# Kernel optimization log

Measured on AMD Instinct MI355X. Metric: run time of the kernel, lower is better.

Reference implementation:

```python
import jax, jax.numpy as jnp
import numpy as np

B, T, H, DH = 4, 2048, 16, 64   # batch, block_size, num_head, chunk_size (per-head dim)
NE = H * DH                      # n_embed = 1024
EPS = 1e-5                       # torch GroupNorm default eps


def _decay_mask(T):
    # D[h, n, m] = gamma_h**(n-m) for n>=m else 0 (RetNet decay matrix)
    gamma = 1.0 - 2.0 ** (-5.0 - jnp.arange(H, dtype=jnp.float32))  # [H]
    idx = jnp.arange(T)
    diff = idx[:, None] - idx[None, :]                # [T, T]
    mask = diff >= 0
    expo = jnp.where(mask, diff, 0).astype(jnp.float32)
    D = (gamma[:, None, None] ** expo[None]) * mask[None].astype(jnp.float32)
    return gamma, D


def setup_inputs() -> dict:
    key = jax.random.key(0)
    ks = jax.random.split(key, 5)
    x = jax.random.normal(ks[0], (B, T, NE), jnp.float32)
    past_kv = jax.random.normal(ks[1], (H, DH, DH), jnp.float32)
    Wq = jax.random.normal(ks[2], (NE, NE), jnp.float32) * 0.02
    Wk = jax.random.normal(ks[3], (NE, NE), jnp.float32) * 0.02
    Wv = jax.random.normal(ks[4], (NE, NE), jnp.float32) * 0.02
    gn_w = jnp.ones((H,), jnp.float32)
    gn_b = jnp.zeros((H,), jnp.float32)
    return {"x": x, "past_kv": past_kv, "Wq": Wq, "Wk": Wk, "Wv": Wv,
            "gn_w": gn_w, "gn_b": gn_b}


def reference(x, past_kv, Wq, Wk, Wv, gn_w, gn_b):
    b, t, c = x.shape
    gamma, D = _decay_mask(t)                                  # [H], [H,T,T]

    def split_heads(y):
        return y.reshape(b, t, H, DH).transpose(0, 2, 1, 3)    # [B,H,T,DH]

    q = split_heads(x @ Wq)
    k = split_heads(x @ Wk)
    v = split_heads(x @ Wv)

    # intra-chunk retention: (Q K^T) * D
    retention = jnp.einsum('bhtd,bhsd->bhts', q, k) * D[None]  # [B,H,T,T]
    inner = jnp.einsum('bhts,bhsd->bhtd', retention, v)        # [B,H,T,DH]

    # cross-chunk term (faithful to source): ((q @ past_kv)^T @ D)^T
    pp = jnp.einsum('bhtd,hde->bhte', q, past_kv)              # [B,H,T,DH]
    cross = jnp.einsum('hst,bhse->bhte', D, pp)                # [B,H,T,DH]

    ret = inner + cross                                        # [B,H,T,DH]

    # GroupNorm(1, H) over channels-first layout [B, H, DH, T]
    y = ret.transpose(0, 1, 3, 2)                              # [B,H,DH,T]
    mu = y.mean(axis=(1, 2, 3), keepdims=True)
    var = y.var(axis=(1, 2, 3), keepdims=True)                 # biased, as torch
    yn = (y - mu) / jnp.sqrt(var + EPS)
    yn = yn * gn_w[None, :, None, None] + gn_b[None, :, None, None]

    # rearrange 'b c h t -> b t (c h)' with (c=H, h=DH)
    out = yn.transpose(0, 3, 1, 2).reshape(b, t, H * DH)       # [B,T,NE]

    # recurrent state update: gamma * past_kv + K^T V, batch-averaged
    current_kv = gamma[:, None, None] * past_kv[None] + \
                 jnp.einsum('bhtd,bhte->bhde', k, v)           # [B,H,DH,DH]
    return out, current_kv.mean(axis=0)
```

## Files before the change

### kernel.cpp

```cpp
#include <hip/hip_runtime.h>
#include <stdint.h>

typedef float v4f __attribute__((ext_vector_type(4)));
typedef short v8s __attribute__((ext_vector_type(8)));

#define SZ_BHTD 8388608
#define SZ_HTD  131072

#define GL2LDS(g, l) __builtin_amdgcn_global_load_lds( \
    (const __attribute__((address_space(1))) void*)(g), \
    (__attribute__((address_space(3))) void*)(l), 16, 0, 0)

__device__ __forceinline__ uint16_t f2bf(float f){
  uint32_t u = __float_as_uint(f);
  u += 0x7fffu + ((u >> 16) & 1u);
  return (uint16_t)(u >> 16);
}
__device__ __forceinline__ float bf2f(uint16_t v){
  return __uint_as_float(((uint32_t)v) << 16);
}

__global__ __launch_bounds__(256) void k_conv(const float* __restrict__ x,
                                              const float* __restrict__ Wq, const float* __restrict__ Wk,
                                              const float* __restrict__ Wv,
                                              uint16_t* __restrict__ xb, uint16_t* __restrict__ wt){
  if (blockIdx.x < 8192){
    int i = blockIdx.x*256 + threadIdx.x;
    const float4 v = ((const float4*)x)[i];
    ushort4 o; o.x = f2bf(v.x); o.y = f2bf(v.y); o.z = f2bf(v.z); o.w = f2bf(v.w);
    ((ushort4*)xb)[i] = o;
    return;
  }
  __shared__ float t[64][65];
  const int blk2 = blockIdx.x - 8192;
  const int z = blk2 >> 8, y = (blk2 >> 4) & 15, xx = blk2 & 15;
  const float* W = z==0 ? Wq : (z==1 ? Wk : Wv);
  int n0 = xx*64, k0 = y*64;
  for (int idx = threadIdx.x; idx < 4096; idx += 256){
    int r = idx >> 6, c = idx & 63;
    t[r][c] = W[(k0+r)*1024 + n0 + c];
  }
  __syncthreads();
  for (int idx = threadIdx.x; idx < 4096; idx += 256){
    int r = idx >> 6, c = idx & 63;
    wt[(size_t)(z*1024 + n0 + r)*1024 + k0 + c] = f2bf(t[c][r]);
  }
}

__global__ __launch_bounds__(256) void k_gemm(const uint16_t* __restrict__ Xb, const uint16_t* __restrict__ Wt,
                                              uint16_t* __restrict__ qkv){
  __shared__ uint16_t As[128*64];
  __shared__ uint16_t Bs[128*64];
  const int tid = threadIdx.x;
  const int lane = tid & 63, w = tid >> 6;
  const int quad = lane >> 4, l16 = lane & 15;
  const int wm = (w >> 1)*64, wn = (w & 1)*64;
  const int bm = blockIdx.x, bn = blockIdx.y;
  v4f acc[4][4] = {};
  const uint16_t* Ag = Xb + (size_t)(bm*128)*1024;
  const uint16_t* Bg = Wt + (size_t)(bn*128)*1024;
  const int rA = lane >> 3;
  const int ce = (((lane & 7) ^ rA) * 8);
  const int xr = l16 & 7;
  for (int k0 = 0; k0 < 1024; k0 += 64){
    #pragma unroll
    for (int j = 0; j < 4; ++j){
      const int cA = w*4 + j;
      const int r = cA*8 + rA;
      GL2LDS(Ag + (size_t)r*1024 + k0 + ce, As + cA*512);
      GL2LDS(Bg + (size_t)r*1024 + k0 + ce, Bs + cA*512);
    }
    __syncthreads();
    #pragma unroll
    for (int kk = 0; kk < 64; kk += 32){
      const int ch = ((quad + (kk >> 3)) ^ xr) * 8;
      v8s a[4], b[4];
      #pragma unroll
      for (int u = 0; u < 4; ++u) a[u] = *(v8s*)&As[(wm + u*16 + l16)*64 + ch];
      #pragma unroll
      for (int u = 0; u < 4; ++u) b[u] = *(v8s*)&Bs[(wn + u*16 + l16)*64 + ch];
      #pragma unroll
      for (int mi = 0; mi < 4; ++mi)
        #pragma unroll
        for (int ni = 0; ni < 4; ++ni)
          acc[mi][ni] = __builtin_amdgcn_mfma_f32_16x16x32_bf16(a[mi], b[ni], acc[mi][ni], 0, 0, 0);
    }
    __syncthreads();
  }
  #pragma unroll
  for (int mi = 0; mi < 4; ++mi){
    #pragma unroll
    for (int ni = 0; ni < 4; ++ni){
      int n = bn*128 + wn + ni*16 + l16;
      int which = n >> 10, cch = n & 1023;
      int hh = cch >> 6, dd = cch & 63;
      #pragma unroll
      for (int r = 0; r < 4; ++r){
        int m = bm*128 + wm + mi*16 + quad*4 + r;
        int b = m >> 11, t = m & 2047;
        qkv[(size_t)which*SZ_BHTD + (size_t)((b*16 + hh)*2048 + t)*64 + dd] = f2bf(acc[mi][ni][r]);
      }
    }
  }
}

__global__ __launch_bounds__(256) void k_pre(const uint16_t* __restrict__ qkv, const float* __restrict__ pkv,
                                             uint16_t* __restrict__ UT, uint16_t* __restrict__ ckp,
                                             float* __restrict__ headv){
  __shared__ uint16_t KTb[64*72];
  __shared__ uint16_t VTb[64*72];
  __shared__ uint16_t VTw[64*72];
  __shared__ float tab[65];
  __shared__ float qbar[64];
  const int tid = threadIdx.x, blk = blockIdx.x;
  const int bh = blk >> 5, c = blk & 31, h = bh & 15;
  const int lane = tid & 63, w = tid >> 6;
  const int quad = lane >> 4, l16 = lane & 15;
  const float g = 1.0f - exp2f(-(float)(5 + h));
  if (tid <= 64) tab[tid] = powf(g, (float)tid);
  const uint16_t* Qg = qkv + (size_t)bh*SZ_HTD + c*4096;
  const uint16_t* Kg = Qg + SZ_BHTD;
  const uint16_t* Vg = Qg + 2*(size_t)SZ_BHTD;
  const float* Pg = pkv + h*4096;
  __syncthreads();
  #pragma unroll
  for (int it = 0; it < 16; ++it){
    int idx = it*256 + tid;
    int s = idx >> 6, d = idx & 63;
    uint16_t kv = Kg[idx], vv = Vg[idx];
    KTb[d*72 + s] = kv;
    VTb[d*72 + s] = vv;
    VTw[d*72 + s] = f2bf(tab[63 - s]*bf2f(vv));
  }
  if (tid < 64){
    float acc = 0.f;
    for (int j = 0; j < 64; ++j) acc = fmaf(tab[j], bf2f(Qg[j*64 + tid]), acc);
    qbar[tid] = acc;
  }
  __syncthreads();
  const int ar = (w*16 + l16)*72 + quad*8;
  v8s aK0 = *(v8s*)&KTb[ar], aK1 = *(v8s*)&KTb[ar + 32];
  v8s aW0 = *(v8s*)&VTw[ar], aW1 = *(v8s*)&VTw[ar + 32];
  v4f accC[4] = {}, accU[4] = {};
  #pragma unroll
  for (int ni = 0; ni < 4; ++ni){
    const int br = (ni*16 + l16)*72 + quad*8;
    v8s bV0 = *(v8s*)&VTb[br], bV1 = *(v8s*)&VTb[br + 32];
    v8s bK0 = *(v8s*)&KTb[br], bK1 = *(v8s*)&KTb[br + 32];
    accC[ni] = __builtin_amdgcn_mfma_f32_16x16x32_bf16(aK0, bV0, accC[ni], 0, 0, 0);
    accC[ni] = __builtin_amdgcn_mfma_f32_16x16x32_bf16(aK1, bV1, accC[ni], 0, 0, 0);
    accU[ni] = __builtin_amdgcn_mfma_f32_16x16x32_bf16(aW0, bK0, accU[ni], 0, 0, 0);
    accU[ni] = __builtin_amdgcn_mfma_f32_16x16x32_bf16(aW1, bK1, accU[ni], 0, 0, 0);
  }
  const size_t ob = (size_t)blk*4096;
  #pragma unroll
  for (int ni = 0; ni < 4; ++ni){
    int e = ni*16 + l16;
    #pragma unroll
    for (int r = 0; r < 4; ++r){
      int d = w*16 + quad*4 + r;
      ckp[ob + d*64 + e] = f2bf(accC[ni][r]);
      UT[ob + d*64 + e]  = f2bf(accU[ni][r]);
    }
  }
  if (tid < 64){
    float acc = 0.f;
    for (int dd = 0; dd < 64; ++dd) acc = fmaf(qbar[dd], Pg[dd*64 + tid], acc);
    headv[(size_t)blk*64 + tid] = acc;
  }
}

__global__ __launch_bounds__(256) void k_scan(const uint16_t* __restrict__ UT, uint16_t* __restrict__ S,
                                              const float* __restrict__ headv, float* __restrict__ tailv){
  if (blockIdx.x < 256){
    const int bh = blockIdx.x >> 2, part = blockIdx.x & 3, h = bh & 15;
    const float g = 1.0f - exp2f(-(float)(5 + h));
    const float g64 = powf(g, 64.0f);
    const int off = part*1024 + threadIdx.x*4;
    float st0=0.f, st1=0.f, st2=0.f, st3=0.f;
    for (int c = 0; c < 32; ++c){
      const size_t base = ((size_t)bh*32 + c)*4096 + off;
      ushort4 u = *(const ushort4*)&UT[base];
      ushort4 o; o.x=f2bf(st0); o.y=f2bf(st1); o.z=f2bf(st2); o.w=f2bf(st3);
      *(ushort4*)&S[base] = o;
      st0 = fmaf(g64, st0, bf2f(u.x)); st1 = fmaf(g64, st1, bf2f(u.y));
      st2 = fmaf(g64, st2, bf2f(u.z)); st3 = fmaf(g64, st3, bf2f(u.w));
    }
    return;
  }
  const int lin = (blockIdx.x - 256)*256 + threadIdx.x;
  const int bh = lin >> 6, e = lin & 63, h = bh & 15;
  const float g = 1.0f - exp2f(-(float)(5 + h));
  const float g64 = powf(g, 64.0f);
  float R = 0.0f;
  for (int c = 31; c >= 0; --c){
    const size_t o = ((size_t)bh*32 + c)*64 + e;
    tailv[o] = R;
    R = fmaf(g64, R, headv[o]);
  }
}

__global__ __launch_bounds__(256) void k_main(const uint16_t* __restrict__ qkv, const uint16_t* __restrict__ Sg_,
                                              const float* __restrict__ pkv, const float* __restrict__ tailv,
                                              uint16_t* __restrict__ ret, float2* __restrict__ pb){
  __shared__ uint16_t Qb[64*72];
  __shared__ uint16_t Kb[64*72];
  __shared__ uint16_t VTb[64*72];
  __shared__ uint16_t B2[64*72];
  __shared__ uint16_t Sb[64*72];
  __shared__ float tab[65];
  __shared__ float ps[8];
  const int tid = threadIdx.x, blk = blockIdx.x;
  const int bh = blk >> 5, c = blk & 31, h = bh & 15;
  const int lane = tid & 63, w = tid >> 6;
  const int quad = lane >> 4, l16 = lane & 15;
  const float g = 1.0f - exp2f(-(float)(5 + h));
  if (tid <= 64) tab[tid] = powf(g, (float)tid);
  const uint16_t* Qg = qkv + (size_t)bh*SZ_HTD + c*4096;
  const uint16_t* Kg = Qg + SZ_BHTD;
  const uint16_t* Vg = Qg + 2*(size_t)SZ_BHTD;
  const uint16_t* Sgp = Sg_ + (size_t)blk*4096;
  const float* Pg = pkv + h*4096;
  #pragma unroll
  for (int v = 0; v < 2; ++v){
    int idx = (tid*2 + v)*8;
    int r = idx >> 6, cc = idx & 63;
    *(uint4*)&Qb[r*72 + cc] = *(const uint4*)&Qg[idx];
    *(uint4*)&Kb[r*72 + cc] = *(const uint4*)&Kg[idx];
    *(uint4*)&Sb[r*72 + cc] = *(const uint4*)&Sgp[idx];
  }
  #pragma unroll
  for (int it = 0; it < 16; ++it){
    int idx = it*256 + tid;
    int r = idx >> 6, cc = idx & 63;
    VTb[cc*72 + r] = Vg[idx];
    B2[cc*72 + r] = f2bf(Pg[idx]);
  }
  __syncthreads();
  const int ar = (w*16 + l16)*72 + quad*8;
  v8s aQ0 = *(v8s*)&Qb[ar], aQ1 = *(v8s*)&Qb[ar + 32];
  v4f accP[4] = {}, accPP[4] = {}, accIT[4] = {};
  #pragma unroll
  for (int ni = 0; ni < 4; ++ni){
    const int br = (ni*16 + l16)*72 + quad*8;
    v8s b0 = *(v8s*)&Kb[br], b1 = *(v8s*)&Kb[br + 32];
    accP[ni] = __builtin_amdgcn_mfma_f32_16x16x32_bf16(aQ0, b0, accP[ni], 0, 0, 0);
    accP[ni] = __builtin_amdgcn_mfma_f32_16x16x32_bf16(aQ1, b1, accP[ni], 0, 0, 0);
    v8s c0 = *(v8s*)&B2[br], c1 = *(v8s*)&B2[br + 32];
    accPP[ni] = __builtin_amdgcn_mfma_f32_16x16x32_bf16(aQ0, c0, accPP[ni], 0, 0, 0);
    accPP[ni] = __builtin_amdgcn_mfma_f32_16x16x32_bf16(aQ1, c1, accPP[ni], 0, 0, 0);
    v8s d0 = *(v8s*)&Sb[br], d1 = *(v8s*)&Sb[br + 32];
    accIT[ni] = __builtin_amdgcn_mfma_f32_16x16x32_bf16(aQ0, d0, accIT[ni], 0, 0, 0);
    accIT[ni] = __builtin_amdgcn_mfma_f32_16x16x32_bf16(aQ1, d1, accIT[ni], 0, 0, 0);
  }
  __syncthreads();
  #pragma unroll
  for (int ni = 0; ni < 4; ++ni){
    #pragma unroll
    for (int r = 0; r < 4; ++r){
      int i = w*16 + quad*4 + r;
      int j = ni*16 + l16;
      Kb[i*72 + j] = f2bf((i >= j) ? accP[ni][r]*tab[i - j] : 0.0f);
      B2[j*72 + i] = f2bf(accPP[ni][r]);
    }
  }
  __syncthreads();
  v8s aP0 = *(v8s*)&Kb[ar], aP1 = *(v8s*)&Kb[ar + 32];
  v8s aM0, aM1;
  {
    int i = w*16 + l16;
    #pragma unroll
    for (int u = 0; u < 8; ++u){
      int j0 = quad*8 + u, j1 = 32 + quad*8 + u;
      aM0[u] = (short)f2bf((j0 >= i) ? tab[j0 - i] : 0.0f);
      aM1[u] = (short)f2bf((j1 >= i) ? tab[j1 - i] : 0.0f);
    }
  }
  v4f accI[4] = {}, accX[4] = {};
  #pragma unroll
  for (int ni = 0; ni < 4; ++ni){
    const int br = (ni*16 + l16)*72 + quad*8;
    v8s b0 = *(v8s*)&VTb[br], b1 = *(v8s*)&VTb[br + 32];
    accI[ni] = __builtin_amdgcn_mfma_f32_16x16x32_bf16(aP0, b0, accI[ni], 0, 0, 0);
    accI[ni] = __builtin_amdgcn_mfma_f32_16x16x32_bf16(aP1, b1, accI[ni], 0, 0, 0);
    v8s e0 = *(v8s*)&B2[br], e1 = *(v8s*)&B2[br + 32];
    accX[ni] = __builtin_amdgcn_mfma_f32_16x16x32_bf16(aM0, e0, accX[ni], 0, 0, 0);
    accX[ni] = __builtin_amdgcn_mfma_f32_16x16x32_bf16(aM1, e1, accX[ni], 0, 0, 0);
  }
  const size_t rbase = (size_t)bh*2048 + (size_t)c*64;
  float s1 = 0.f, s2 = 0.f;
  #pragma unroll
  for (int ni = 0; ni < 4; ++ni){
    int d = ni*16 + l16;
    float tl = tailv[(size_t)blk*64 + d];
    #pragma unroll
    for (int r = 0; r < 4; ++r){
      int i = w*16 + quad*4 + r;
      float v = accI[ni][r] + tab[i + 1]*accIT[ni][r] + accX[ni][r] + tab[64 - i]*tl;
      ret[(rbase + i)*64 + d] = f2bf(v);
      s1 += v; s2 += v*v;
    }
  }
  #pragma unroll
  for (int off = 32; off > 0; off >>= 1){
    s1 += __shfl_down(s1, off);
    s2 += __shfl_down(s2, off);
  }
  if (lane == 0){ ps[w*2] = s1; ps[w*2+1] = s2; }
  __syncthreads();
  if (tid == 0){
    float2 o; o.x = ps[0] + ps[2] + ps[4] + ps[6];
    o.y = ps[1] + ps[3] + ps[5] + ps[7];
    pb[blk] = o;
  }
}

__global__ __launch_bounds__(256) void k_stats(const float2* __restrict__ pb, float* __restrict__ stats){
  __shared__ float ps[8];
  const int b = blockIdx.x;
  float s = 0.0f, s2 = 0.0f;
  for (int i = threadIdx.x; i < 512; i += 256){
    const float2 p = pb[(size_t)b*512 + i];
    s += p.x; s2 += p.y;
  }
  #pragma unroll
  for (int off = 32; off > 0; off >>= 1){
    s  += __shfl_down(s, off);
    s2 += __shfl_down(s2, off);
  }
  const int wv = threadIdx.x >> 6;
  if ((threadIdx.x & 63) == 0){ ps[wv*2] = s; ps[wv*2+1] = s2; }
  __syncthreads();
  if (threadIdx.x == 0){
    stats[b*2]   = ps[0] + ps[2] + ps[4] + ps[6];
    stats[b*2+1] = ps[1] + ps[3] + ps[5] + ps[7];
  }
}

__global__ __launch_bounds__(256) void k_norm(const uint16_t* __restrict__ ret, const float* __restrict__ stats,
                                              const float* __restrict__ gw, const float* __restrict__ gb,
                                              float* __restrict__ out){
  const int o = (blockIdx.x*256 + threadIdx.x)*4;
  const int b = o >> 21, t = (o >> 10) & 2047, cch = o & 1023;
  const int h = cch >> 6, d = cch & 63;
  const float inv = 1.0f/2097152.0f;
  const float mu = stats[b*2]*inv;
  const float var = stats[b*2+1]*inv - mu*mu;
  const float rs = rsqrtf(var + 1e-5f);
  const float w = gw[h]*rs, bb = gb[h];
  const ushort4 v = *(const ushort4*)&ret[((size_t)(b*16 + h)*2048 + t)*64 + d];
  float4 r;
  r.x = (bf2f(v.x) - mu)*w + bb; r.y = (bf2f(v.y) - mu)*w + bb;
  r.z = (bf2f(v.z) - mu)*w + bb; r.w = (bf2f(v.w) - mu)*w + bb;
  *(float4*)&out[o] = r;
}

__global__ __launch_bounds__(256) void k_ckb(const float* __restrict__ pkv, const uint16_t* __restrict__ ckp,
                                             float* __restrict__ out2){
  const int lin = blockIdx.x*256 + threadIdx.x;
  const int i = lin*4;
  const int h = i >> 12, de = i & 4095;
  const float g = 1.0f - exp2f(-(float)(5 + h));
  float acc[4] = {0.0f, 0.0f, 0.0f, 0.0f};
  for (int b = 0; b < 4; ++b){
    const uint16_t* base = ckp + ((size_t)(b*16 + h)*32)*4096 + de;
    for (int c = 0; c < 32; ++c){
      #pragma unroll
      for (int u = 0; u < 4; ++u) acc[u] += bf2f(base[(size_t)c*4096 + u]);
    }
  }
  #pragma unroll
  for (int u = 0; u < 4; ++u)
    out2[i + u] = fmaf(g, pkv[i + u], 0.25f*acc[u]);
}

extern "C" void kernel_launch(void* const* d_in, const int* in_sizes, int n_in,
                              void* d_out, int out_size, void* d_ws, size_t ws_size,
                              hipStream_t stream){
  const float* x   = (const float*)d_in[0];
  const float* pkv = (const float*)d_in[1];
  const float* Wq  = (const float*)d_in[2];
  const float* Wk  = (const float*)d_in[3];
  const float* Wv  = (const float*)d_in[4];
  const float* gnw = (const float*)d_in[5];
  const float* gnb = (const float*)d_in[6];
  float* out  = (float*)d_out;
  float* out2 = out + 8388608;

  char* ws = (char*)d_ws;
  size_t off = 0;
  float*    stats = (float*)(ws + off);    off += 256;
  float2*   pb    = (float2*)(ws + off);   off += (size_t)8192*8;
  uint16_t* Xb    = (uint16_t*)(ws + off); off += (size_t)8388608*2;
  uint16_t* Wt    = (uint16_t*)(ws + off); off += (size_t)3145728*2;
  uint16_t* QKV   = (uint16_t*)(ws + off); off += (size_t)3*8388608*2;
  uint16_t* ret   = (uint16_t*)(ws + off); off += (size_t)8388608*2;
  uint16_t* UT    = (uint16_t*)(ws + off); off += (size_t)8388608*2;
  uint16_t* S     = (uint16_t*)(ws + off); off += (size_t)8388608*2;
  uint16_t* CKp   = (uint16_t*)(ws + off); off += (size_t)8388608*2;
  float*    headv = (float*)(ws + off);    off += (size_t)131072*4;
  float*    tailv = (float*)(ws + off);    off += (size_t)131072*4;

  k_conv<<<8960, 256, 0, stream>>>(x, Wq, Wk, Wv, Xb, Wt);
  k_gemm<<<dim3(64, 24), 256, 0, stream>>>(Xb, Wt, QKV);
  k_pre<<<2048, 256, 0, stream>>>(QKV, pkv, UT, CKp, headv);
  k_scan<<<272, 256, 0, stream>>>(UT, S, headv, tailv);
  k_main<<<2048, 256, 0, stream>>>(QKV, S, pkv, tailv, ret, pb);
  k_stats<<<4, 256, 0, stream>>>(pb, stats);
  k_norm<<<8192, 256, 0, stream>>>(ret, stats, gnw, gnb, out);
  k_ckb<<<64, 256, 0, stream>>>(pkv, CKp, out2);
}
```

Baseline: 252.5 us.

## Rewrite QKV GEMM as 256x256 double-buffered tile with 8 waves; spread k_ckb

The QKV projection GEMM moves from 128x128 tiles with 4 waves to 256x256 tiles with 8 waves. LDS is double-buffered, so the global-to-LDS loads for tile k+2 overlap the MFMA work on the current tile, using explicit vmcnt waits, raw barriers and s_setprio around the MFMA bursts. The aim is more data reuse per tile and hiding load latency, at the cost of far fewer blocks (384), more LDS and more registers. k_ckb is also relaunched as 256 blocks of 64 threads to spread its reduction over more CUs.

```diff
diff --git a/kernel.cpp b/kernel.cpp
--- a/kernel.cpp
+++ b/kernel.cpp
@@ -10,6 +10,8 @@
 #define GL2LDS(g, l) __builtin_amdgcn_global_load_lds( \
     (const __attribute__((address_space(1))) void*)(g), \
     (__attribute__((address_space(3))) void*)(l), 16, 0, 0)
+
+#define BAR() do{ asm volatile("" ::: "memory"); __builtin_amdgcn_s_barrier(); asm volatile("" ::: "memory"); }while(0)
 
 __device__ __forceinline__ uint16_t f2bf(float f){
   uint32_t u = __float_as_uint(f);
@@ -47,58 +49,97 @@
   }
 }
 
-__global__ __launch_bounds__(256) void k_gemm(const uint16_t* __restrict__ Xb, const uint16_t* __restrict__ Wt,
-                                              uint16_t* __restrict__ qkv){
-  __shared__ uint16_t As[128*64];
-  __shared__ uint16_t Bs[128*64];
+#define NT 16
+__global__ __launch_bounds__(512, 2) void k_gemm(const uint16_t* __restrict__ Xb, const uint16_t* __restrict__ Wt,
+                                                 uint16_t* __restrict__ qkv){
+  __shared__ uint16_t As[2][256*64];
+  __shared__ uint16_t Bs[2][256*64];
   const int tid = threadIdx.x;
   const int lane = tid & 63, w = tid >> 6;
   const int quad = lane >> 4, l16 = lane & 15;
-  const int wm = (w >> 1)*64, wn = (w & 1)*64;
+  const int wm = w >> 2, wn = w & 3;
   const int bm = blockIdx.x, bn = blockIdx.y;
-  v4f acc[4][4] = {};
-  const uint16_t* Ag = Xb + (size_t)(bm*128)*1024;
-  const uint16_t* Bg = Wt + (size_t)(bn*128)*1024;
+  const uint16_t* Ag = Xb + (size_t)(bm*256)*1024;
+  const uint16_t* Bg = Wt + (size_t)(bn*256)*1024;
   const int rA = lane >> 3;
   const int ce = (((lane & 7) ^ rA) * 8);
   const int xr = l16 & 7;
-  for (int k0 = 0; k0 < 1024; k0 += 64){
-    #pragma unroll
-    for (int j = 0; j < 4; ++j){
-      const int cA = w*4 + j;
-      const int r = cA*8 + rA;
-      GL2LDS(Ag + (size_t)r*1024 + k0 + ce, As + cA*512);
-      GL2LDS(Bg + (size_t)r*1024 + k0 + ce, Bs + cA*512);
-    }
-    __syncthreads();
-    #pragma unroll
-    for (int kk = 0; kk < 64; kk += 32){
-      const int ch = ((quad + (kk >> 3)) ^ xr) * 8;
-      v8s a[4], b[4];
+  const int c0 = (quad ^ xr) * 8;
+  const int c1 = ((quad + 4) ^ xr) * 8;
+  const int abase = (wm*128 + l16)*64;
+  const int bbase = (wn*64 + l16)*64;
+  v4f acc[8][4] = {};
+
+#define STAGE(kt, buf) do{ \
+    const int _k0 = (kt)*64; \
+    _Pragma("unroll") \
+    for (int _j = 0; _j < 4; ++_j){ \
+      const int _row = _j*64 + w*8; \
+      GL2LDS(Ag + (size_t)(_row + rA)*1024 + _k0 + ce, &As[buf][_row*64]); \
+      GL2LDS(Bg + (size_t)(_row + rA)*1024 + _k0 + ce, &Bs[buf][_row*64]); \
+    } \
+  }while(0)
+
+  STAGE(0, 0);
+  STAGE(1, 1);
+  asm volatile("s_waitcnt vmcnt(8)" ::: "memory");
+  BAR();
+
+  #pragma unroll 2
+  for (int t = 0; t < NT; ++t){
+    const int cur = t & 1;
+    const uint16_t* Asb = As[cur];
+    const uint16_t* Bsb = Bs[cur];
+    #pragma unroll
+    for (int q = 0; q < 4; ++q){
+      const int mh = q >> 1, nh = q & 1;
+      v8s a0[4], a1[4], b0[2], b1[2];
       #pragma unroll
-      for (int u = 0; u < 4; ++u) a[u] = *(v8s*)&As[(wm + u*16 + l16)*64 + ch];
+      for (int im = 0; im < 4; ++im){
+        const int ro = abase + (mh*64 + im*16)*64;
+        a0[im] = *(const v8s*)&Asb[ro + c0];
+        a1[im] = *(const v8s*)&Asb[ro + c1];
+      }
       #pragma unroll
-      for (int u = 0; u < 4; ++u) b[u] = *(v8s*)&Bs[(wn + u*16 + l16)*64 + ch];
+      for (int in = 0; in < 2; ++in){
+        const int ro = bbase + (nh*32 + in*16)*64;
+        b0[in] = *(const v8s*)&Bsb[ro + c0];
+        b1[in] = *(const v8s*)&Bsb[ro + c1];
+      }
+      BAR();
+      __builtin_amdgcn_s_setprio(1);
       #pragma unroll
-      for (int mi = 0; mi < 4; ++mi)
+      for (int im = 0; im < 4; ++im){
         #pragma unroll
-        for (int ni = 0; ni < 4; ++ni)
-          acc[mi][ni] = __builtin_amdgcn_mfma_f32_16x16x32_bf16(a[mi], b[ni], acc[mi][ni], 0, 0, 0);
-    }
-    __syncthreads();
-  }
-  #pragma unroll
-  for (int mi = 0; mi < 4; ++mi){
+        for (int in = 0; in < 2; ++in){
+          acc[mh*4+im][nh*2+in] = __builtin_amdgcn_mfma_f32_16x16x32_bf16(a0[im], b0[in], acc[mh*4+im][nh*2+in], 0, 0, 0);
+          acc[mh*4+im][nh*2+in] = __builtin_amdgcn_mfma_f32_16x16x32_bf16(a1[im], b1[in], acc[mh*4+im][nh*2+in], 0, 0, 0);
+        }
+      }
+      __builtin_amdgcn_s_setprio(0);
+      BAR();
+    }
+    if (t < NT-2) STAGE(t+2, cur);
+    if (t < NT-1){
+      if (t < NT-2){ asm volatile("s_waitcnt vmcnt(8)" ::: "memory"); }
+      else         { asm volatile("s_waitcnt vmcnt(0)" ::: "memory"); }
+      BAR();
+    }
+  }
+#undef STAGE
+
+  #pragma unroll
+  for (int mi = 0; mi < 8; ++mi){
     #pragma unroll
     for (int ni = 0; ni < 4; ++ni){
-      int n = bn*128 + wn + ni*16 + l16;
+      int n = bn*256 + wn*64 + ni*16 + l16;
       int which = n >> 10, cch = n & 1023;
       int hh = cch >> 6, dd = cch & 63;
       #pragma unroll
       for (int r = 0; r < 4; ++r){
-        int m = bm*128 + wm + mi*16 + quad*4 + r;
-        int b = m >> 11, t = m & 2047;
-        qkv[(size_t)which*SZ_BHTD + (size_t)((b*16 + hh)*2048 + t)*64 + dd] = f2bf(acc[mi][ni][r]);
+        int m = bm*256 + wm*128 + mi*16 + quad*4 + r;
+        int b = m >> 11, tt = m & 2047;
+        qkv[(size_t)which*SZ_BHTD + (size_t)((b*16 + hh)*2048 + tt)*64 + dd] = f2bf(acc[mi][ni][r]);
       }
     }
   }
@@ -355,9 +396,9 @@
   *(float4*)&out[o] = r;
 }
 
-__global__ __launch_bounds__(256) void k_ckb(const float* __restrict__ pkv, const uint16_t* __restrict__ ckp,
-                                             float* __restrict__ out2){
-  const int lin = blockIdx.x*256 + threadIdx.x;
+__global__ __launch_bounds__(64) void k_ckb(const float* __restrict__ pkv, const uint16_t* __restrict__ ckp,
+                                            float* __restrict__ out2){
+  const int lin = blockIdx.x*64 + threadIdx.x;
   const int i = lin*4;
   const int h = i >> 12, de = i & 4095;
   const float g = 1.0f - exp2f(-(float)(5 + h));
@@ -402,11 +443,11 @@
   float*    tailv = (float*)(ws + off);    off += (size_t)131072*4;
 
   k_conv<<<8960, 256, 0, stream>>>(x, Wq, Wk, Wv, Xb, Wt);
-  k_gemm<<<dim3(64, 24), 256, 0, stream>>>(Xb, Wt, QKV);
+  k_gemm<<<dim3(32, 12), 512, 0, stream>>>(Xb, Wt, QKV);
   k_pre<<<2048, 256, 0, stream>>>(QKV, pkv, UT, CKp, headv);
   k_scan<<<272, 256, 0, stream>>>(UT, S, headv, tailv);
   k_main<<<2048, 256, 0, stream>>>(QKV, S, pkv, tailv, ret, pb);
   k_stats<<<4, 256, 0, stream>>>(pb, stats);
   k_norm<<<8192, 256, 0, stream>>>(ret, stats, gnw, gnb, out);
-  k_ckb<<<64, 256, 0, stream>>>(pkv, CKp, out2);
-}
+  k_ckb<<<256, 64, 0, stream>>>(pkv, CKp, out2);
+}
```

After: 279.1 us. 10.5% more time.
